# Optimization experiments

Hardware: AMD Instinct MI355X
Metric: run time of the kernel (lower is better)

The kernel has to match this reference:

```python
import jax, jax.numpy as jnp
import numpy as np

B, T, C = 1, 2048, 2048
H, KH, HD = 16, 4, 128  # n_head, n_kv_head, head_dim
ROPE_BASE = 10000.0


def setup_inputs() -> dict:
    key = jax.random.key(0)
    ks = jax.random.split(key, 5)
    s = 0.02
    return {
        "x": jax.random.normal(ks[0], (B, T, C), jnp.float32),
        "Wq": jax.random.normal(ks[1], (C, H * HD), jnp.float32) * s,
        "Wk": jax.random.normal(ks[2], (C, KH * HD), jnp.float32) * s,
        "Wv": jax.random.normal(ks[3], (C, KH * HD), jnp.float32) * s,
        "Wo": jax.random.normal(ks[4], (H * HD, C), jnp.float32) * s,
        "position_ids": jnp.arange(T, dtype=jnp.int32),
    }


def _rotate_half(a):
    h = a.shape[-1] // 2
    return jnp.concatenate([-a[..., h:], a[..., :h]], axis=-1)


def reference(x, Wq, Wk, Wv, Wo, position_ids):
    b, t, c = x.shape
    n_rep = H // KH
    # projections -> [B, heads, T, HD]
    q = (x @ Wq).reshape(b, t, H, HD).transpose(0, 2, 1, 3)
    k = (x @ Wk).reshape(b, t, KH, HD).transpose(0, 2, 1, 3)
    v = (x @ Wv).reshape(b, t, KH, HD).transpose(0, 2, 1, 3)
    # rotary embedding cache [T, HD]
    inv_freq = 1.0 / (ROPE_BASE ** (jnp.arange(0, HD, 2, dtype=jnp.float32) / HD))
    pos = jnp.arange(t, dtype=jnp.float32)
    freqs = pos[:, None] * inv_freq[None, :]
    emb = jnp.concatenate([freqs, freqs], axis=-1)
    cos = jnp.cos(emb)[position_ids][None, None]  # [1,1,T,HD]
    sin = jnp.sin(emb)[position_ids][None, None]
    q = q * cos + _rotate_half(q) * sin
    k = k * cos + _rotate_half(k) * sin
    # GQA: group query heads instead of materializing repeated K/V
    qg = q.reshape(b, KH, n_rep, t, HD)
    scale = jnp.float32(1.0 / np.sqrt(HD))
    scores = jnp.einsum('bgrtd,bgsd->bgrts', qg, k) * scale
    causal = jnp.tril(jnp.ones((t, t), dtype=bool))
    scores = jnp.where(causal, scores, jnp.float32(-1e30))
    p = jax.nn.softmax(scores, axis=-1)
    y = jnp.einsum('bgrts,bgsd->bgrtd', p, v)
    y = y.reshape(b, H, t, HD).transpose(0, 2, 1, 3).reshape(b, t, H * HD)
    return y @ Wo
```

## Files before the change

### kernel.cpp

```cpp
#include <hip/hip_runtime.h>

typedef unsigned short u16;
using bf16x8 = __attribute__((ext_vector_type(8))) short;
using f32x4  = __attribute__((ext_vector_type(4))) float;

#define GLD16(g, l)                                                            \
  __builtin_amdgcn_global_load_lds(                                            \
      (const __attribute__((address_space(1))) void*)(g),                      \
      (__attribute__((address_space(3))) void*)(l), 16, 0, 0)

__device__ __forceinline__ u16 f2b(float x) {
  union { float f; unsigned u; } v; v.f = x;
  unsigned r = v.u + 0x7FFF + ((v.u >> 16) & 1);
  return (u16)(r >> 16);
}
__device__ __forceinline__ float b2f(u16 x) {
  union { unsigned u; float f; } v; v.u = (unsigned)x << 16; return v.f;
}

__global__ void cast_bf16_kernel(const float* __restrict__ in,
                                 u16* __restrict__ out, int n4,
                                 const int* __restrict__ pos,
                                 float2* __restrict__ tbl) {
  int gid = blockIdx.x * blockDim.x + threadIdx.x;
  int stride = gridDim.x * blockDim.x;
  const float c0 = -0.015625f * 13.287712379549449f;
  for (int j = gid; j < 2048 * 64; j += stride) {
    int t = j >> 6, d = j & 63;
    float ang = (float)pos[t] * exp2f((float)d * c0);
    tbl[j] = make_float2(cosf(ang), sinf(ang));
  }
  for (int i = gid; i < n4; i += stride) {
    float4 v = ((const float4*)in)[i];
    ushort4 o;
    o.x = f2b(v.x); o.y = f2b(v.y); o.z = f2b(v.z); o.w = f2b(v.w);
    ((ushort4*)out)[i] = o;
  }
}

__global__ void transpose_all_w_kernel(const float* __restrict__ Wq,
                                       const float* __restrict__ Wk,
                                       const float* __restrict__ Wv,
                                       const float* __restrict__ Wo,
                                       u16* __restrict__ Wqkv_bt,
                                       u16* __restrict__ Wo_bt) {
  __shared__ float tile[32][33];
  const int bx = blockIdx.x, k0 = blockIdx.y * 32;
  const int tx = threadIdx.x, ty = threadIdx.y;
  const float* src; int srcN, n0s; u16* dst; int dstRow0;
  if (bx < 64)      { src = Wq; srcN = 2048; n0s = bx * 32;        dst = Wqkv_bt; dstRow0 = bx * 32; }
  else if (bx < 80) { src = Wk; srcN = 512;  n0s = (bx - 64) * 32; dst = Wqkv_bt; dstRow0 = 2048 + (bx - 64) * 32; }
  else if (bx < 96) { src = Wv; srcN = 512;  n0s = (bx - 80) * 32; dst = Wqkv_bt; dstRow0 = 2560 + (bx - 80) * 32; }
  else              { src = Wo; srcN = 2048; n0s = (bx - 96) * 32; dst = Wo_bt;   dstRow0 = (bx - 96) * 32; }
#pragma unroll
  for (int r = 0; r < 4; r++)
    tile[ty + r * 8][tx] = src[(size_t)(k0 + ty + r * 8) * srcN + n0s + tx];
  __syncthreads();
#pragma unroll
  for (int r = 0; r < 4; r++)
    dst[(size_t)(dstRow0 + ty + r * 8) * 2048 + k0 + tx] = f2b(tile[tx][ty + r * 8]);
}

__global__ void transpose_v_kernel(const u16* __restrict__ src,
                                   u16* __restrict__ dst) {
  __shared__ u16 tile[32][33];
  int h = blockIdx.z;
  int t0 = blockIdx.x * 32, d0 = blockIdx.y * 32;
  const u16* s = src + (size_t)h * 2048 * 128;
  u16* d = dst + (size_t)h * 128 * 2048;
  int tx = threadIdx.x, ty = threadIdx.y;
#pragma unroll
  for (int r = 0; r < 4; r++)
    tile[ty + r * 8][tx] = s[(size_t)(t0 + ty + r * 8) * 128 + d0 + tx];
  __syncthreads();
#pragma unroll
  for (int r = 0; r < 4; r++)
    d[(size_t)(d0 + ty + r * 8) * 2048 + t0 + tx] = tile[tx][ty + r * 8];
}

__global__ __launch_bounds__(256, 2)
void gemm_qkv_rope(const u16* __restrict__ A, const u16* __restrict__ Bt,
                   const float2* __restrict__ tbl, u16* __restrict__ Qb,
                   u16* __restrict__ Kb, u16* __restrict__ Vb) {
  __shared__ u16 lds_[8][128 * 32];
  const int K = 2048;
  const int tid = threadIdx.x;
  const int lane = tid & 63;
  const int w = tid >> 6;
  const int wr = w >> 1, wc = w & 1;
  const int m0 = blockIdx.y * 128, n0 = blockIdx.x * 128;

  f32x4 acc[4][4] = {};

  const int srow = tid >> 2, skg = tid & 3;
  const u16* Ag0 = A + (size_t)(m0 + srow) * K + skg * 8;
  const u16* Ag1 = A + (size_t)(m0 + 64 + srow) * K + skg * 8;
  const u16* Bg0 = Bt + (size_t)(n0 + srow) * K + skg * 8;
  const u16* Bg1 = Bt + (size_t)(n0 + 64 + srow) * K + skg * 8;

  const int l0 = tid * 8, l1 = (256 + tid) * 8;
  u16 *pa0 = lds_[0], *pa1 = lds_[1], *pa2 = lds_[2], *pa3 = lds_[3];
  u16 *pb0 = lds_[4], *pb1 = lds_[5], *pb2 = lds_[6], *pb3 = lds_[7];

#define GSTAGE(k0v, pa, pb)                                                    \
  {                                                                            \
    GLD16(Ag0 + (k0v), (pa) + l0);                                             \
    GLD16(Ag1 + (k0v), (pa) + l1);                                             \
    GLD16(Bg0 + (k0v), (pb) + l0);                                             \
    GLD16(Bg1 + (k0v), (pb) + l1);                                             \
  }

  GSTAGE(0, pa0, pb0);
  GSTAGE(32, pa1, pb1);

  const int frow = lane & 15, fk = (lane >> 4) * 8;
  const int nk = K >> 5;

  for (int i = 0; i < nk; ++i) {
    if (i + 2 < nk) {
      GSTAGE((i + 2) * 32, pa2, pb2);
      asm volatile("s_waitcnt vmcnt(8)" ::: "memory");
    } else if (i + 1 < nk) {
      asm volatile("s_waitcnt vmcnt(4)" ::: "memory");
    } else {
      asm volatile("s_waitcnt vmcnt(0)" ::: "memory");
    }
    __builtin_amdgcn_s_barrier();
    __builtin_amdgcn_sched_barrier(0);
    bf16x8 av[4], bv[4];
#pragma unroll
    for (int m = 0; m < 4; m++)
      av[m] = *(const bf16x8*)(pa0 + (wr * 64 + m * 16 + frow) * 32 + fk);
#pragma unroll
    for (int n = 0; n < 4; n++)
      bv[n] = *(const bf16x8*)(pb0 + (wc * 64 + n * 16 + frow) * 32 + fk);
#pragma unroll
    for (int m = 0; m < 4; m++)
#pragma unroll
      for (int n = 0; n < 4; n++)
        acc[m][n] =
            __builtin_amdgcn_mfma_f32_16x16x32_bf16(av[m], bv[n], acc[m][n], 0, 0, 0);
    u16* t;
    t = pa0; pa0 = pa1; pa1 = pa2; pa2 = pa3; pa3 = t;
    t = pb0; pb0 = pb1; pb1 = pb2; pb2 = pb3; pb3 = t;
  }
#undef GSTAGE

  const int crow = (lane >> 4) * 4, ccol = lane & 15;
  if (n0 < 2560) {
    __syncthreads();
    float* S = (float*)lds_;
#pragma unroll
    for (int m = 0; m < 4; m++)
#pragma unroll
      for (int n = 0; n < 4; n++)
#pragma unroll
        for (int r = 0; r < 4; r++)
          S[(wr * 64 + m * 16 + crow + r) * 128 + wc * 64 + n * 16 + ccol] =
              acc[m][n][r];
    __syncthreads();
    const bool isQ = (n0 < 2048);
    u16* dst = isQ ? Qb + (size_t)(n0 >> 7) * 2048 * 128
                   : Kb + (size_t)((n0 - 2048) >> 7) * 2048 * 128;
    const float sgn = (wc == 0) ? -1.f : 1.f;
    const float qs = isQ ? 0.08838834764831845f : 1.0f;
#pragma unroll
    for (int m = 0; m < 4; m++)
#pragma unroll
      for (int n = 0; n < 4; n++)
#pragma unroll
        for (int r = 0; r < 4; r++) {
          int row = wr * 64 + m * 16 + crow + r;
          int col = wc * 64 + n * 16 + ccol;
          int t = m0 + row, d = col & 63;
          float2 cs = tbl[t * 64 + d];
          float val = acc[m][n][r] * cs.x + sgn * S[row * 128 + (col ^ 64)] * cs.y;
          dst[(size_t)t * 128 + col] = f2b(val * qs);
        }
  } else {
    u16* dst = Vb + (size_t)((n0 - 2560) >> 7) * 2048 * 128;
#pragma unroll
    for (int m = 0; m < 4; m++)
#pragma unroll
      for (int n = 0; n < 4; n++)
#pragma unroll
        for (int r = 0; r < 4; r++) {
          int row = wr * 64 + m * 16 + crow + r;
          int col = wc * 64 + n * 16 + ccol;
          dst[(size_t)(m0 + row) * 128 + col] = f2b(acc[m][n][r]);
        }
  }
}

__global__ __launch_bounds__(256, 2)
void gemm_bt_128(const u16* __restrict__ A, const u16* __restrict__ Bt,
                 float* __restrict__ C, int M, int N, int K) {
  __shared__ u16 As[4][128 * 32];
  __shared__ u16 Bs[4][128 * 32];
  const int tid = threadIdx.x;
  const int lane = tid & 63;
  const int w = tid >> 6;
  const int wr = w >> 1, wc = w & 1;
  const int m0 = blockIdx.y * 128, n0 = blockIdx.x * 128;

  f32x4 acc[4][4] = {};

  const int srow = tid >> 2, skg = tid & 3;
  const u16* Ag0 = A + (size_t)(m0 + srow) * K + skg * 8;
  const u16* Ag1 = A + (size_t)(m0 + 64 + srow) * K + skg * 8;
  const u16* Bg0 = Bt + (size_t)(n0 + srow) * K + skg * 8;
  const u16* Bg1 = Bt + (size_t)(n0 + 64 + srow) * K + skg * 8;

  const int l0 = tid * 8, l1 = (256 + tid) * 8;
  u16 *pa0 = As[0], *pa1 = As[1], *pa2 = As[2], *pa3 = As[3];
  u16 *pb0 = Bs[0], *pb1 = Bs[1], *pb2 = Bs[2], *pb3 = Bs[3];

#define GSTAGE(k0v, pa, pb)                                                    \
  {                                                                            \
    GLD16(Ag0 + (k0v), (pa) + l0);                                             \
    GLD16(Ag1 + (k0v), (pa) + l1);                                             \
    GLD16(Bg0 + (k0v), (pb) + l0);                                             \
    GLD16(Bg1 + (k0v), (pb) + l1);                                             \
  }

  GSTAGE(0, pa0, pb0);
  GSTAGE(32, pa1, pb1);

  const int frow = lane & 15, fk = (lane >> 4) * 8;
  const int nk = K >> 5;

  for (int i = 0; i < nk; ++i) {
    if (i + 2 < nk) {
      GSTAGE((i + 2) * 32, pa2, pb2);
      asm volatile("s_waitcnt vmcnt(8)" ::: "memory");
    } else if (i + 1 < nk) {
      asm volatile("s_waitcnt vmcnt(4)" ::: "memory");
    } else {
      asm volatile("s_waitcnt vmcnt(0)" ::: "memory");
    }
    __builtin_amdgcn_s_barrier();
    __builtin_amdgcn_sched_barrier(0);
    bf16x8 av[4], bv[4];
#pragma unroll
    for (int m = 0; m < 4; m++)
      av[m] = *(const bf16x8*)(pa0 + (wr * 64 + m * 16 + frow) * 32 + fk);
#pragma unroll
    for (int n = 0; n < 4; n++)
      bv[n] = *(const bf16x8*)(pb0 + (wc * 64 + n * 16 + frow) * 32 + fk);
#pragma unroll
    for (int m = 0; m < 4; m++)
#pragma unroll
      for (int n = 0; n < 4; n++)
        acc[m][n] =
            __builtin_amdgcn_mfma_f32_16x16x32_bf16(av[m], bv[n], acc[m][n], 0, 0, 0);
    u16* t;
    t = pa0; pa0 = pa1; pa1 = pa2; pa2 = pa3; pa3 = t;
    t = pb0; pb0 = pb1; pb1 = pb2; pb2 = pb3; pb3 = t;
  }
#undef GSTAGE

  const int crow = (lane >> 4) * 4, ccol = lane & 15;
#pragma unroll
  for (int m = 0; m < 4; m++)
#pragma unroll
    for (int n = 0; n < 4; n++)
#pragma unroll
      for (int r = 0; r < 4; r++)
        C[(size_t)(m0 + wr * 64 + m * 16 + crow + r) * N +
          (n0 + wc * 64 + n * 16 + ccol)] = acc[m][n][r];
}

__global__ __launch_bounds__(256, 2)
void attn_kernel(const u16* __restrict__ Qb, const u16* __restrict__ Kb,
                 const u16* __restrict__ Vtb, u16* __restrict__ Op,
                 float* __restrict__ ml) {
  __shared__ u16 Ks[2][64 * 128];
  __shared__ u16 Vs[2][128 * 64];
  __shared__ u16 Ps[4][16 * 64];
  const int tid = threadIdx.x, lane = tid & 63, w = tid >> 6;
  const int h = blockIdx.y, g = h >> 2;
  const int z = blockIdx.z;
  const int frow = lane & 15, fgrp = lane >> 4;
  const int t0 = blockIdx.x;
  const int t1 = 31 - t0;
  const int c0 = (t0 >= z) ? ((t0 - z) >> 1) + 1 : 0;
  const int c1 = ((t1 - z) >> 1) + 1;
  const int nit = c0 + c1;

  const u16* Kg = Kb + (size_t)g * 2048 * 128;
  const u16* Vg = Vtb + (size_t)g * 128 * 2048;

#define STAGE(j0v, B)                                                          \
  {                                                                            \
    _Pragma("unroll")                                                          \
    for (int i = 0; i < 4; i++) {                                              \
      int p = tid + i * 256;                                                   \
      int kr = p >> 4, kc = (p & 15) ^ (kr & 7);                               \
      GLD16(Kg + (size_t)((j0v) + kr) * 128 + kc * 8, &Ks[B][p * 8]);          \
      int vr = p >> 3, vc = (p & 7) ^ (vr & 7);                                \
      GLD16(Vg + (size_t)vr * 2048 + (j0v) + vc * 8, &Vs[B][p * 8]);           \
    }                                                                          \
  }

#define FLUSH()                                                                \
  {                                                                            \
    _Pragma("unroll")                                                          \
    for (int r = 0; r < 4; r++) {                                              \
      float inv = lrow[r] > 0.f ? 1.0f / lrow[r] : 0.f;                        \
      int t = qw + fgrp * 4 + r;                                               \
      _Pragma("unroll")                                                        \
      for (int db = 0; db < 8; db++)                                           \
        Op[(size_t)z * 4194304 + (size_t)t * 2048 + h * 128 + db * 16 + frow] =\
            f2b(o[db][r] * inv);                                               \
      if (frow == 0) {                                                         \
        int mi = (((z * 16 + h) * 2048) + t) * 2;                              \
        ml[mi] = mrow[r]; ml[mi + 1] = lrow[r];                                \
      }                                                                        \
    }                                                                          \
  }

  int qw = t0 * 64 + w * 16;
  bf16x8 qf[4];
  {
    const u16* Qrow = Qb + ((size_t)h * 2048 + (qw + frow)) * 128 + fgrp * 8;
#pragma unroll
    for (int kf = 0; kf < 4; kf++) qf[kf] = *(const bf16x8*)(Qrow + kf * 32);
  }

  f32x4 o[8] = {};
  float mrow[4], lrow[4];
#pragma unroll
  for (int r = 0; r < 4; r++) { mrow[r] = -1e30f; lrow[r] = 0.f; }

  STAGE(z * 64, 0);
  __syncthreads();

  for (int it = 0; it < nit; ++it) {
    const int buf = it & 1;
    if (it + 1 < nit) {
      const int itn = it + 1;
      const int jn = (itn < c0) ? z + 2 * itn : z + 2 * (itn - c0);
      STAGE(jn * 64, buf ^ 1);
    }
    if (it == c0) {
      FLUSH();
#pragma unroll
      for (int db = 0; db < 8; db++)
#pragma unroll
        for (int r = 0; r < 4; r++) o[db][r] = 0.f;
#pragma unroll
      for (int r = 0; r < 4; r++) { mrow[r] = -1e30f; lrow[r] = 0.f; }
      qw = t1 * 64 + w * 16;
      const u16* Qrow = Qb + ((size_t)h * 2048 + (qw + frow)) * 128 + fgrp * 8;
#pragma unroll
      for (int kf = 0; kf < 4; kf++) qf[kf] = *(const bf16x8*)(Qrow + kf * 32);
    }
    const int pass = (it < c0) ? 0 : 1;
    const int j = (pass == 0) ? z + 2 * it : z + 2 * (it - c0);
    const bool diag = (pass == 0) ? (j == t0) : (j == t1);

    f32x4 sc[4] = {};
#pragma unroll
    for (int c = 0; c < 4; c++)
#pragma unroll
      for (int kf = 0; kf < 4; kf++) {
        int row = c * 16 + frow;
        bf16x8 kv = *(const bf16x8*)(
            &Ks[buf][row * 128 + ((kf * 4 + fgrp) ^ (row & 7)) * 8]);
        sc[c] = __builtin_amdgcn_mfma_f32_16x16x32_bf16(qf[kf], kv, sc[c], 0, 0, 0);
      }
    if (diag) {
#pragma unroll
      for (int c = 0; c < 4; c++) {
        int jj = c * 16 + frow;
#pragma unroll
        for (int r = 0; r < 4; r++)
          if (jj > (w * 16 + fgrp * 4 + r)) sc[c][r] = -1e30f;
      }
    }
    float pm[4];
#pragma unroll
    for (int r = 0; r < 4; r++)
      pm[r] = fmaxf(fmaxf(sc[0][r], sc[1][r]), fmaxf(sc[2][r], sc[3][r]));
#pragma unroll
    for (int off = 1; off < 16; off <<= 1)
#pragma unroll
      for (int r = 0; r < 4; r++) pm[r] = fmaxf(pm[r], __shfl_xor(pm[r], off, 64));
    bool nd = false;
#pragma unroll
    for (int r = 0; r < 4; r++) nd = nd || (pm[r] > mrow[r] + 8.f);
    if (__any(nd)) {
#pragma unroll
      for (int r = 0; r < 4; r++) {
        float mn = fmaxf(mrow[r], pm[r]);
        float alpha = __expf(mrow[r] - mn);
        mrow[r] = mn;
        lrow[r] *= alpha;
#pragma unroll
        for (int db = 0; db < 8; db++) o[db][r] *= alpha;
      }
    }
    float rs[4];
#pragma unroll
    for (int r = 0; r < 4; r++) {
      float s = 0.f;
#pragma unroll
      for (int c = 0; c < 4; c++) { sc[c][r] = __expf(sc[c][r] - mrow[r]); s += sc[c][r]; }
      rs[r] = s;
    }
#pragma unroll
    for (int off = 1; off < 16; off <<= 1)
#pragma unroll
      for (int r = 0; r < 4; r++) rs[r] += __shfl_xor(rs[r], off, 64);
#pragma unroll
    for (int r = 0; r < 4; r++) lrow[r] += rs[r];
    u16* Pw = Ps[w];
#pragma unroll
    for (int c = 0; c < 4; c++)
#pragma unroll
      for (int r = 0; r < 4; r++) {
        int row = fgrp * 4 + r, col = c * 16 + frow;
        Pw[row * 64 + (((col >> 3) ^ row) & 7) * 8 + (col & 7)] = f2b(sc[c][r]);
      }
    asm volatile("s_waitcnt lgkmcnt(0)" ::: "memory");
    bf16x8 pf[2];
#pragma unroll
    for (int ks = 0; ks < 2; ks++)
      pf[ks] = *(const bf16x8*)(
          &Pw[frow * 64 + ((ks * 4 + fgrp) ^ (frow & 7)) * 8]);
#pragma unroll
    for (int db = 0; db < 8; db++)
#pragma unroll
      for (int ks = 0; ks < 2; ks++) {
        int row = db * 16 + frow;
        bf16x8 vf = *(const bf16x8*)(
            &Vs[buf][row * 64 + ((ks * 4 + fgrp) ^ (row & 7)) * 8]);
        o[db] = __builtin_amdgcn_mfma_f32_16x16x32_bf16(pf[ks], vf, o[db], 0, 0, 0);
      }
    __syncthreads();
  }
  FLUSH();
#undef STAGE
#undef FLUSH
}

__global__ void attn_combine_kernel(const u16* __restrict__ Op,
                                    const float* __restrict__ ml,
                                    u16* __restrict__ Y) {
  int u = blockIdx.x * blockDim.x + threadIdx.x;
  int t = u >> 4, h = u & 15;
  int i0 = ((0 * 16 + h) * 2048 + t) * 2;
  int i1 = ((1 * 16 + h) * 2048 + t) * 2;
  float m0 = ml[i0], l0 = ml[i0 + 1];
  float m1 = ml[i1], l1 = ml[i1 + 1];
  float m = fmaxf(m0, m1);
  float w0 = __expf(m0 - m) * l0, w1 = __expf(m1 - m) * l1;
  float inv = 1.0f / (w0 + w1);
  w0 *= inv; w1 *= inv;
  size_t base = (size_t)t * 2048 + h * 128;
#pragma unroll
  for (int i = 0; i < 16; i++) {
    bf16x8 a = *(const bf16x8*)(Op + base + i * 8);
    bf16x8 b = *(const bf16x8*)(Op + 4194304 + base + i * 8);
    bf16x8 out;
#pragma unroll
    for (int jj = 0; jj < 8; jj++)
      out[jj] = (short)f2b(w0 * b2f((u16)a[jj]) + w1 * b2f((u16)b[jj]));
    *(bf16x8*)(Y + base + i * 8) = out;
  }
}

extern "C" void kernel_launch(void* const* d_in, const int* in_sizes, int n_in,
                              void* d_out, int out_size, void* d_ws,
                              size_t ws_size, hipStream_t stream) {
  const float* x  = (const float*)d_in[0];
  const float* Wq = (const float*)d_in[1];
  const float* Wk = (const float*)d_in[2];
  const float* Wv = (const float*)d_in[3];
  const float* Wo = (const float*)d_in[4];
  const int* pos  = (const int*)d_in[5];
  float* out = (float*)d_out;
  char* ws = (char*)d_ws;

  u16* xb      = (u16*)(ws + 0);
  u16* Wqkv_bt = (u16*)(ws + 8388608);
  u16* Wo_bt   = (u16*)(ws + 20971520);
  float2* tbl  = (float2*)(ws + 29360128);
  u16* Yb      = (u16*)(ws + 31457280);
  u16* Qb      = (u16*)(ws + 54525952);
  u16* Kb      = (u16*)(ws + 62914560);
  u16* Vb      = (u16*)(ws + 65011712);
  u16* Vtb     = (u16*)(ws + 67108864);
  u16* Op      = (u16*)(ws + 0);
  float* ml    = (float*)(ws + 16777216);

  cast_bf16_kernel<<<1024, 256, 0, stream>>>(x, xb, 2048 * 2048 / 4, pos, tbl);
  transpose_all_w_kernel<<<dim3(160, 64), dim3(32, 8), 0, stream>>>(
      Wq, Wk, Wv, Wo, Wqkv_bt, Wo_bt);

  gemm_qkv_rope<<<dim3(24, 16), 256, 0, stream>>>(xb, Wqkv_bt, tbl, Qb, Kb, Vb);

  transpose_v_kernel<<<dim3(64, 4, 4), dim3(32, 8), 0, stream>>>(Vb, Vtb);

  attn_kernel<<<dim3(16, 16, 2), 256, 0, stream>>>(Qb, Kb, Vtb, Op, ml);
  attn_combine_kernel<<<128, 256, 0, stream>>>(Op, ml, Yb);

  gemm_bt_128<<<dim3(2048 / 128, 2048 / 128), 256, 0, stream>>>(Yb, Wo_bt, out, 2048, 2048, 2048);
}
```

Before: 242.2 us.

## Fuse prep kernels, write transposed V from QKV GEMM, split attention three ways

```diff
diff --git a/kernel.cpp b/kernel.cpp
--- a/kernel.cpp
+++ b/kernel.cpp
@@ -18,70 +18,52 @@
   union { unsigned u; float f; } v; v.u = (unsigned)x << 16; return v.f;
 }
 
-__global__ void cast_bf16_kernel(const float* __restrict__ in,
-                                 u16* __restrict__ out, int n4,
-                                 const int* __restrict__ pos,
-                                 float2* __restrict__ tbl) {
-  int gid = blockIdx.x * blockDim.x + threadIdx.x;
-  int stride = gridDim.x * blockDim.x;
-  const float c0 = -0.015625f * 13.287712379549449f;
-  for (int j = gid; j < 2048 * 64; j += stride) {
-    int t = j >> 6, d = j & 63;
-    float ang = (float)pos[t] * exp2f((float)d * c0);
-    tbl[j] = make_float2(cosf(ang), sinf(ang));
-  }
-  for (int i = gid; i < n4; i += stride) {
-    float4 v = ((const float4*)in)[i];
-    ushort4 o;
-    o.x = f2b(v.x); o.y = f2b(v.y); o.z = f2b(v.z); o.w = f2b(v.w);
-    ((ushort4*)out)[i] = o;
-  }
-}
-
-__global__ void transpose_all_w_kernel(const float* __restrict__ Wq,
-                                       const float* __restrict__ Wk,
-                                       const float* __restrict__ Wv,
-                                       const float* __restrict__ Wo,
-                                       u16* __restrict__ Wqkv_bt,
-                                       u16* __restrict__ Wo_bt) {
+__global__ void prep_kernel(const float* __restrict__ x,
+                            const float* __restrict__ Wq,
+                            const float* __restrict__ Wk,
+                            const float* __restrict__ Wv,
+                            const float* __restrict__ Wo,
+                            const int* __restrict__ pos, u16* __restrict__ xb,
+                            float2* __restrict__ tbl, u16* __restrict__ Wqkv_bt,
+                            u16* __restrict__ Wo_bt) {
   __shared__ float tile[32][33];
-  const int bx = blockIdx.x, k0 = blockIdx.y * 32;
-  const int tx = threadIdx.x, ty = threadIdx.y;
-  const float* src; int srcN, n0s; u16* dst; int dstRow0;
-  if (bx < 64)      { src = Wq; srcN = 2048; n0s = bx * 32;        dst = Wqkv_bt; dstRow0 = bx * 32; }
-  else if (bx < 80) { src = Wk; srcN = 512;  n0s = (bx - 64) * 32; dst = Wqkv_bt; dstRow0 = 2048 + (bx - 64) * 32; }
-  else if (bx < 96) { src = Wv; srcN = 512;  n0s = (bx - 80) * 32; dst = Wqkv_bt; dstRow0 = 2560 + (bx - 80) * 32; }
-  else              { src = Wo; srcN = 2048; n0s = (bx - 96) * 32; dst = Wo_bt;   dstRow0 = (bx - 96) * 32; }
-#pragma unroll
-  for (int r = 0; r < 4; r++)
-    tile[ty + r * 8][tx] = src[(size_t)(k0 + ty + r * 8) * srcN + n0s + tx];
-  __syncthreads();
-#pragma unroll
-  for (int r = 0; r < 4; r++)
-    dst[(size_t)(dstRow0 + ty + r * 8) * 2048 + k0 + tx] = f2b(tile[tx][ty + r * 8]);
-}
-
-__global__ void transpose_v_kernel(const u16* __restrict__ src,
-                                   u16* __restrict__ dst) {
-  __shared__ u16 tile[32][33];
-  int h = blockIdx.z;
-  int t0 = blockIdx.x * 32, d0 = blockIdx.y * 32;
-  const u16* s = src + (size_t)h * 2048 * 128;
-  u16* d = dst + (size_t)h * 128 * 2048;
-  int tx = threadIdx.x, ty = threadIdx.y;
-#pragma unroll
-  for (int r = 0; r < 4; r++)
-    tile[ty + r * 8][tx] = s[(size_t)(t0 + ty + r * 8) * 128 + d0 + tx];
-  __syncthreads();
-#pragma unroll
-  for (int r = 0; r < 4; r++)
-    d[(size_t)(d0 + ty + r * 8) * 2048 + t0 + tx] = tile[tx][ty + r * 8];
+  const int b = blockIdx.x, tid = threadIdx.x;
+  if (b < 10240) {
+    const int bx = b % 160, k0 = (b / 160) * 32;
+    const int tx = tid & 31, ty = tid >> 5;
+    const float* src; int srcN, n0s; u16* dst; int dstRow0;
+    if (bx < 64)      { src = Wq; srcN = 2048; n0s = bx * 32;        dst = Wqkv_bt; dstRow0 = bx * 32; }
+    else if (bx < 80) { src = Wk; srcN = 512;  n0s = (bx - 64) * 32; dst = Wqkv_bt; dstRow0 = 2048 + (bx - 64) * 32; }
+    else if (bx < 96) { src = Wv; srcN = 512;  n0s = (bx - 80) * 32; dst = Wqkv_bt; dstRow0 = 2560 + (bx - 80) * 32; }
+    else              { src = Wo; srcN = 2048; n0s = (bx - 96) * 32; dst = Wo_bt;   dstRow0 = (bx - 96) * 32; }
+#pragma unroll
+    for (int r = 0; r < 4; r++)
+      tile[ty + r * 8][tx] = src[(size_t)(k0 + ty + r * 8) * srcN + n0s + tx];
+    __syncthreads();
+#pragma unroll
+    for (int r = 0; r < 4; r++)
+      dst[(size_t)(dstRow0 + ty + r * 8) * 2048 + k0 + tx] = f2b(tile[tx][ty + r * 8]);
+  } else {
+    int gid = (b - 10240) * 256 + tid;
+    const float c0 = -0.015625f * 13.287712379549449f;
+    for (int j = gid; j < 2048 * 64; j += 262144) {
+      int t = j >> 6, d = j & 63;
+      float ang = (float)pos[t] * exp2f((float)d * c0);
+      tbl[j] = make_float2(cosf(ang), sinf(ang));
+    }
+    for (int i = gid; i < 1048576; i += 262144) {
+      float4 v = ((const float4*)x)[i];
+      ushort4 o;
+      o.x = f2b(v.x); o.y = f2b(v.y); o.z = f2b(v.z); o.w = f2b(v.w);
+      ((ushort4*)xb)[i] = o;
+    }
+  }
 }
 
 __global__ __launch_bounds__(256, 2)
 void gemm_qkv_rope(const u16* __restrict__ A, const u16* __restrict__ Bt,
                    const float2* __restrict__ tbl, u16* __restrict__ Qb,
-                   u16* __restrict__ Kb, u16* __restrict__ Vb) {
+                   u16* __restrict__ Kb, u16* __restrict__ Vtb) {
   __shared__ u16 lds_[8][128 * 32];
   const int K = 2048;
   const int tid = threadIdx.x;
@@ -147,18 +129,18 @@
 #undef GSTAGE
 
   const int crow = (lane >> 4) * 4, ccol = lane & 15;
+  __syncthreads();
+  float* S = (float*)lds_;
+#pragma unroll
+  for (int m = 0; m < 4; m++)
+#pragma unroll
+    for (int n = 0; n < 4; n++)
+#pragma unroll
+      for (int r = 0; r < 4; r++)
+        S[(wr * 64 + m * 16 + crow + r) * 128 + wc * 64 + n * 16 + ccol] =
+            acc[m][n][r];
+  __syncthreads();
   if (n0 < 2560) {
-    __syncthreads();
-    float* S = (float*)lds_;
-#pragma unroll
-    for (int m = 0; m < 4; m++)
-#pragma unroll
-      for (int n = 0; n < 4; n++)
-#pragma unroll
-        for (int r = 0; r < 4; r++)
-          S[(wr * 64 + m * 16 + crow + r) * 128 + wc * 64 + n * 16 + ccol] =
-              acc[m][n][r];
-    __syncthreads();
     const bool isQ = (n0 < 2048);
     u16* dst = isQ ? Qb + (size_t)(n0 >> 7) * 2048 * 128
                    : Kb + (size_t)((n0 - 2048) >> 7) * 2048 * 128;
@@ -178,17 +160,16 @@
           dst[(size_t)t * 128 + col] = f2b(val * qs);
         }
   } else {
-    u16* dst = Vb + (size_t)((n0 - 2560) >> 7) * 2048 * 128;
-#pragma unroll
-    for (int m = 0; m < 4; m++)
-#pragma unroll
-      for (int n = 0; n < 4; n++)
-#pragma unroll
-        for (int r = 0; r < 4; r++) {
-          int row = wr * 64 + m * 16 + crow + r;
-          int col = wc * 64 + n * 16 + ccol;
-          dst[(size_t)(m0 + row) * 128 + col] = f2b(acc[m][n][r]);
-        }
+    const int g = (n0 - 2560) >> 7;
+    u16* dst = Vtb + (size_t)g * 128 * 2048;
+    const int d = tid >> 1, th = (tid & 1) * 64;
+#pragma unroll
+    for (int j = 0; j < 8; j++) {
+      bf16x8 v;
+#pragma unroll
+      for (int e = 0; e < 8; e++) v[e] = (short)f2b(S[(th + j * 8 + e) * 128 + d]);
+      *(bf16x8*)(dst + (size_t)d * 2048 + m0 + th + j * 8) = v;
+    }
   }
 }
 
@@ -270,12 +251,13 @@
           (n0 + wc * 64 + n * 16 + ccol)] = acc[m][n][r];
 }
 
-__global__ __launch_bounds__(256, 2)
+__global__ __launch_bounds__(256, 3)
 void attn_kernel(const u16* __restrict__ Qb, const u16* __restrict__ Kb,
-                 const u16* __restrict__ Vtb, u16* __restrict__ Op,
+                 const u16* __restrict__ Vtb, u16* __restrict__ op0,
+                 u16* __restrict__ op1, u16* __restrict__ op2,
                  float* __restrict__ ml) {
-  __shared__ u16 Ks[2][64 * 128];
-  __shared__ u16 Vs[2][128 * 64];
+  __shared__ u16 Ks[64 * 128];
+  __shared__ u16 Vs[128 * 64];
   __shared__ u16 Ps[4][16 * 64];
   const int tid = threadIdx.x, lane = tid & 63, w = tid >> 6;
   const int h = blockIdx.y, g = h >> 2;
@@ -283,22 +265,23 @@
   const int frow = lane & 15, fgrp = lane >> 4;
   const int t0 = blockIdx.x;
   const int t1 = 31 - t0;
-  const int c0 = (t0 >= z) ? ((t0 - z) >> 1) + 1 : 0;
-  const int c1 = ((t1 - z) >> 1) + 1;
+  const int c0 = (t0 >= z) ? (t0 - z) / 3 + 1 : 0;
+  const int c1 = (t1 - z) / 3 + 1;
   const int nit = c0 + c1;
+  u16* myOp = (z == 0) ? op0 : (z == 1) ? op1 : op2;
 
   const u16* Kg = Kb + (size_t)g * 2048 * 128;
   const u16* Vg = Vtb + (size_t)g * 128 * 2048;
 
-#define STAGE(j0v, B)                                                          \
+#define STAGE(j0v)                                                             \
   {                                                                            \
     _Pragma("unroll")                                                          \
     for (int i = 0; i < 4; i++) {                                              \
       int p = tid + i * 256;                                                   \
       int kr = p >> 4, kc = (p & 15) ^ (kr & 7);                               \
-      GLD16(Kg + (size_t)((j0v) + kr) * 128 + kc * 8, &Ks[B][p * 8]);          \
+      GLD16(Kg + (size_t)((j0v) + kr) * 128 + kc * 8, Ks + p * 8);             \
       int vr = p >> 3, vc = (p & 7) ^ (vr & 7);                                \
-      GLD16(Vg + (size_t)vr * 2048 + (j0v) + vc * 8, &Vs[B][p * 8]);           \
+      GLD16(Vg + (size_t)vr * 2048 + (j0v) + vc * 8, Vs + p * 8);              \
     }                                                                          \
   }
 
@@ -310,8 +293,7 @@
       int t = qw + fgrp * 4 + r;                                               \
       _Pragma("unroll")                                                        \
       for (int db = 0; db < 8; db++)                                           \
-        Op[(size_t)z * 4194304 + (size_t)t * 2048 + h * 128 + db * 16 + frow] =\
-            f2b(o[db][r] * inv);                                               \
+        myOp[(size_t)t * 2048 + h * 128 + db * 16 + frow] = f2b(o[db][r] * inv);\
       if (frow == 0) {                                                         \
         int mi = (((z * 16 + h) * 2048) + t) * 2;                              \
         ml[mi] = mrow[r]; ml[mi + 1] = lrow[r];                                \
@@ -332,16 +314,10 @@
 #pragma unroll
   for (int r = 0; r < 4; r++) { mrow[r] = -1e30f; lrow[r] = 0.f; }
 
-  STAGE(z * 64, 0);
-  __syncthreads();
-
   for (int it = 0; it < nit; ++it) {
-    const int buf = it & 1;
-    if (it + 1 < nit) {
-      const int itn = it + 1;
-      const int jn = (itn < c0) ? z + 2 * itn : z + 2 * (itn - c0);
-      STAGE(jn * 64, buf ^ 1);
-    }
+    const int pass = (it < c0) ? 0 : 1;
+    const int j = (pass == 0) ? z + 3 * it : z + 3 * (it - c0);
+    STAGE(j * 64);
     if (it == c0) {
       FLUSH();
 #pragma unroll
@@ -355,8 +331,7 @@
 #pragma unroll
       for (int kf = 0; kf < 4; kf++) qf[kf] = *(const bf16x8*)(Qrow + kf * 32);
     }
-    const int pass = (it < c0) ? 0 : 1;
-    const int j = (pass == 0) ? z + 2 * it : z + 2 * (it - c0);
+    __syncthreads();
     const bool diag = (pass == 0) ? (j == t0) : (j == t1);
 
     f32x4 sc[4] = {};
@@ -366,7 +341,7 @@
       for (int kf = 0; kf < 4; kf++) {
         int row = c * 16 + frow;
         bf16x8 kv = *(const bf16x8*)(
-            &Ks[buf][row * 128 + ((kf * 4 + fgrp) ^ (row & 7)) * 8]);
+            &Ks[row * 128 + ((kf * 4 + fgrp) ^ (row & 7)) * 8]);
         sc[c] = __builtin_amdgcn_mfma_f32_16x16x32_bf16(qf[kf], kv, sc[c], 0, 0, 0);
       }
     if (diag) {
@@ -434,7 +409,7 @@
       for (int ks = 0; ks < 2; ks++) {
         int row = db * 16 + frow;
         bf16x8 vf = *(const bf16x8*)(
-            &Vs[buf][row * 64 + ((ks * 4 + fgrp) ^ (row & 7)) * 8]);
+            &Vs[row * 64 + ((ks * 4 + fgrp) ^ (row & 7)) * 8]);
         o[db] = __builtin_amdgcn_mfma_f32_16x16x32_bf16(pf[ks], vf, o[db], 0, 0, 0);
       }
     __syncthreads();
@@ -444,28 +419,31 @@
 #undef FLUSH
 }
 
-__global__ void attn_combine_kernel(const u16* __restrict__ Op,
+__global__ void attn_combine_kernel(const u16* __restrict__ op0,
+                                    const u16* __restrict__ op1,
+                                    const u16* __restrict__ op2,
                                     const float* __restrict__ ml,
                                     u16* __restrict__ Y) {
   int u = blockIdx.x * blockDim.x + threadIdx.x;
   int t = u >> 4, h = u & 15;
-  int i0 = ((0 * 16 + h) * 2048 + t) * 2;
-  int i1 = ((1 * 16 + h) * 2048 + t) * 2;
-  float m0 = ml[i0], l0 = ml[i0 + 1];
-  float m1 = ml[i1], l1 = ml[i1 + 1];
-  float m = fmaxf(m0, m1);
-  float w0 = __expf(m0 - m) * l0, w1 = __expf(m1 - m) * l1;
-  float inv = 1.0f / (w0 + w1);
-  w0 *= inv; w1 *= inv;
+  float m0 = ml[((0 + h) * 2048 + t) * 2],       l0 = ml[((0 + h) * 2048 + t) * 2 + 1];
+  float m1 = ml[((16 + h) * 2048 + t) * 2],      l1 = ml[((16 + h) * 2048 + t) * 2 + 1];
+  float m2 = ml[((32 + h) * 2048 + t) * 2],      l2 = ml[((32 + h) * 2048 + t) * 2 + 1];
+  float m = fmaxf(fmaxf(m0, m1), m2);
+  float w0 = __expf(m0 - m) * l0, w1 = __expf(m1 - m) * l1, w2 = __expf(m2 - m) * l2;
+  float inv = 1.0f / (w0 + w1 + w2);
+  w0 *= inv; w1 *= inv; w2 *= inv;
   size_t base = (size_t)t * 2048 + h * 128;
 #pragma unroll
   for (int i = 0; i < 16; i++) {
-    bf16x8 a = *(const bf16x8*)(Op + base + i * 8);
-    bf16x8 b = *(const bf16x8*)(Op + 4194304 + base + i * 8);
+    bf16x8 a = *(const bf16x8*)(op0 + base + i * 8);
+    bf16x8 b = *(const bf16x8*)(op1 + base + i * 8);
+    bf16x8 c = *(const bf16x8*)(op2 + base + i * 8);
     bf16x8 out;
 #pragma unroll
     for (int jj = 0; jj < 8; jj++)
-      out[jj] = (short)f2b(w0 * b2f((u16)a[jj]) + w1 * b2f((u16)b[jj]));
+      out[jj] = (short)f2b(w0 * b2f((u16)a[jj]) + w1 * b2f((u16)b[jj]) +
+                           w2 * b2f((u16)c[jj]));
     *(bf16x8*)(Y + base + i * 8) = out;
   }
 }
@@ -487,23 +465,21 @@
   u16* Wo_bt   = (u16*)(ws + 20971520);
   float2* tbl  = (float2*)(ws + 29360128);
   u16* Yb      = (u16*)(ws + 31457280);
+  u16* Op2     = (u16*)(ws + 39845888);
   u16* Qb      = (u16*)(ws + 54525952);
   u16* Kb      = (u16*)(ws + 62914560);
-  u16* Vb      = (u16*)(ws + 65011712);
   u16* Vtb     = (u16*)(ws + 67108864);
-  u16* Op      = (u16*)(ws + 0);
+  u16* Op0     = (u16*)(ws + 0);
+  u16* Op1     = (u16*)(ws + 8388608);
   float* ml    = (float*)(ws + 16777216);
 
-  cast_bf16_kernel<<<1024, 256, 0, stream>>>(x, xb, 2048 * 2048 / 4, pos, tbl);
-  transpose_all_w_kernel<<<dim3(160, 64), dim3(32, 8), 0, stream>>>(
-      Wq, Wk, Wv, Wo, Wqkv_bt, Wo_bt);
-
-  gemm_qkv_rope<<<dim3(24, 16), 256, 0, stream>>>(xb, Wqkv_bt, tbl, Qb, Kb, Vb);
-
-  transpose_v_kernel<<<dim3(64, 4, 4), dim3(32, 8), 0, stream>>>(Vb, Vtb);
-
-  attn_kernel<<<dim3(16, 16, 2), 256, 0, stream>>>(Qb, Kb, Vtb, Op, ml);
-  attn_combine_kernel<<<128, 256, 0, stream>>>(Op, ml, Yb);
-
-  gemm_bt_128<<<dim3(2048 / 128, 2048 / 128), 256, 0, stream>>>(Yb, Wo_bt, out, 2048, 2048, 2048);
-}
+  prep_kernel<<<11264, 256, 0, stream>>>(x, Wq, Wk, Wv, Wo, pos, xb, tbl,
+                                         Wqkv_bt, Wo_bt);
+
+  gemm_qkv_rope<<<dim3(24, 16), 256, 0, stream>>>(xb, Wqkv_bt, tbl, Qb, Kb, Vtb);
+
+  attn_kernel<<<dim3(16, 16, 3), 256, 0, stream>>>(Qb, Kb, Vtb, Op0, Op1, Op2, ml);
+  attn_combine_kernel<<<128, 256, 0, stream>>>(Op0, Op1, Op2, ml, Yb);
+
+  gemm_bt_128<<<dim3(16, 16), 256, 0, stream>>>(Yb, Wo_bt, out, 2048, 2048, 2048);
+}
```

Measured after the change: 243.1 us. About the same (+0.4%).
